# Kernel tuning notes

Hardware: AMD Instinct MI355X
Metric: run time of the kernel (lower is better)

## Reference

```python
import jax, jax.numpy as jnp
import numpy as np

# Fixed MANO structural constants (from MANO_RIGHT.pkl)
PARENTS = np.array([-1, 0, 1, 2, 0, 4, 5, 0, 7, 8, 0, 10, 11, 0, 13, 14])
FINGERTIP = np.array([745, 333, 444, 555, 672])
REMAP = np.array([0, 13, 14, 15, 16, 1, 2, 3, 17, 4, 5, 6, 18, 10, 11, 12, 19, 7, 8, 9, 20])
NV, NJ, NB, NP = 778, 16, 10, 135  # verts, joints, shape betas, pose-basis dim


def setup_inputs() -> dict:
    key = jax.random.key(0)
    ks = jax.random.split(key, 9)
    B = 8192
    beta = jax.random.normal(ks[0], (B, NB), jnp.float32)
    pose = jax.random.normal(ks[1], (B, NJ - 1, 3), jnp.float32) * 0.3
    rvec = jax.random.normal(ks[2], (B, 3), jnp.float32) * 0.3
    tvec = jax.random.normal(ks[3], (B, 3), jnp.float32)
    V = jax.random.normal(ks[4], (NV, 3), jnp.float32) * 0.1          # v_template
    S = jax.random.normal(ks[5], (NV, 3, NB), jnp.float32) * 0.01     # shapedirs
    P = jax.random.normal(ks[6], (NP, NV * 3), jnp.float32) * 0.01    # posedirs (reshaped, transposed)
    J_reg = jax.random.uniform(ks[7], (NJ, NV), jnp.float32)
    J_reg = J_reg / jnp.sum(J_reg, axis=-1, keepdims=True)
    W = jax.random.uniform(ks[8], (NV, NJ), jnp.float32)
    W = W / jnp.sum(W, axis=-1, keepdims=True)                        # skinning weights
    return {"beta": beta, "pose": pose, "rvec": rvec, "tvec": tvec,
            "V": V, "S": S, "P": P, "J_reg": J_reg, "W": W}


def _rodrigues(r):
    # r: [..., 3] axis-angle -> [..., 3, 3] rotation matrices
    sq = jnp.sum(r * r, axis=-1, keepdims=True)
    angle = jnp.sqrt(sq + 1e-8)
    axis = r / angle
    cos = jnp.cos(angle)[..., None]
    sin = jnp.sin(angle)[..., None]
    x, y, z = axis[..., 0], axis[..., 1], axis[..., 2]
    zeros = jnp.zeros_like(x)
    K = jnp.stack([zeros, -z, y, z, zeros, -x, -y, x, zeros], axis=-1)
    K = K.reshape(r.shape[:-1] + (3, 3))
    outer = axis[..., :, None] * axis[..., None, :]
    eye = jnp.eye(3, dtype=r.dtype)
    return cos * eye + (1.0 - cos) * outer + sin * K


def reference(beta, pose, rvec, tvec, V, S, P, J_reg, W):
    B = beta.shape[0]
    dtype = beta.dtype
    full_pose = jnp.concatenate([rvec[:, None, :], pose], axis=1)          # [B,16,3]
    # shape blendshapes
    v_shaped = V + jnp.einsum('bl,vkl->bvk', beta, S)                      # [B,778,3]
    Jrest = jnp.einsum('jv,bvk->bjk', J_reg, v_shaped)                     # [B,16,3]
    # pose blendshapes
    rot = _rodrigues(full_pose)                                            # [B,16,3,3]
    pose_feat = (rot[:, 1:] - jnp.eye(3, dtype=dtype)).reshape(B, NP)      # [B,135]
    v_posed = v_shaped + jnp.matmul(pose_feat, P).reshape(B, NV, 3)        # [B,778,3]
    # rigid transforms along the kinematic chain
    rel = Jrest.at[:, 1:].add(-Jrest[:, PARENTS[1:]])                      # parent-relative joint offsets
    T = jnp.zeros((B, NJ, 4, 4), dtype=dtype)
    T = T.at[..., :3, :3].set(rot).at[..., :3, 3].set(rel).at[..., 3, 3].set(1.0)
    chain = [T[:, 0]]
    for i in range(1, NJ):
        chain.append(jnp.matmul(chain[int(PARENTS[i])], T[:, i]))
    A = jnp.stack(chain, axis=1)                                           # [B,16,4,4] world transforms
    posed_joints = A[..., :3, 3]                                           # [B,16,3]
    # relative-to-rest transforms: A_rel = A - pad(A @ [Jrest;0])
    corr = jnp.einsum('bjmn,bjn->bjm', A[..., :3, :3], Jrest)
    A_rel = A.at[..., :3, 3].add(-corr)
    # linear blend skinning
    Tv = jnp.einsum('vj,bjmn->bvmn', W, A_rel)                             # [B,778,4,4]
    verts = jnp.einsum('bvmn,bvn->bvm', Tv[..., :3, :3], v_posed) + Tv[..., :3, 3]
    # 16 joints + 5 fingertips, remapped to 21 joints
    joints = jnp.concatenate([posed_joints, verts[:, FINGERTIP]], axis=1)[:, REMAP]
    verts = verts + tvec[:, None, :]
    joints = joints + tvec[:, None, :]
    return verts, joints
```

## Files before the change

kernel.cpp:

```cpp
#include <hip/hip_runtime.h>
#include <hip/hip_bf16.h>

typedef __attribute__((ext_vector_type(8))) short short8v;
typedef __attribute__((ext_vector_type(4))) float float4v;

#define BATCH 8192
#define NVERT 778
#define NJOINT 16
#define NPOSE 135
#define KEXT  160
#define NVT   52

#define WSB_JS    0u
#define WSB_PFX   4096u
#define WSB_A     (WSB_PFX  + 2621440u)
#define WSB_PTXF  (WSB_A    + 6291456u)
#define WSB_WF    (WSB_PTXF + 798720u)
#define WSB_ATF   (WSB_WF   + 53248u)

__global__ __launch_bounds__(256) void prep_kernel(
    const float* __restrict__ S, const float* __restrict__ V,
    const float* __restrict__ J_reg, const float* __restrict__ P,
    const float* __restrict__ W,
    float* __restrict__ wsJS, __hip_bfloat16* __restrict__ PtxF,
    __hip_bfloat16* __restrict__ WF)
{
    if (blockIdx.x < 132) {
        int o = blockIdx.x * 4 + (threadIdx.x >> 6);
        int lane = threadIdx.x & 63;
        float s = 0.f;
        if (o < 480) {
            int j = o / 30, k = (o / 10) % 3, l = o % 10;
            for (int v = lane; v < NVERT; v += 64)
                s += J_reg[j * NVERT + v] * S[v * 30 + k * 10 + l];
        } else if (o < 528) {
            int o2 = o - 480;
            int j = o2 / 3, k = o2 % 3;
            for (int v = lane; v < NVERT; v += 64)
                s += J_reg[j * NVERT + v] * V[v * 3 + k];
        }
#pragma unroll
        for (int m = 32; m >= 1; m >>= 1) s += __shfl_xor(s, m, 64);
        if (lane == 0 && o < 528) wsJS[o] = s;
        return;
    }

    int idx = (blockIdx.x - 132) * 256 + threadIdx.x;
    if (idx < NVT * 3 * 5 * 64) {
        int vt = idx / 960;
        int rem = idx % 960;
        int k = rem / 320;
        int rem2 = rem % 320;
        int kc = rem2 / 64;
        int lane = rem2 % 64;
        int v = vt * 16 + (lane & 15);
        int kbase = kc * 32 + (lane >> 4) * 8;
        short8v out;
#pragma unroll
        for (int jj = 0; jj < 8; ++jj) {
            int kk = kbase + jj;
            float val = 0.f;
            if (v < NVERT) {
                if (kk < NPOSE)            val = P[(size_t)kk * (NVERT * 3) + v * 3 + k];
                else if (kk < NPOSE + 10)  val = S[v * 30 + k * 10 + (kk - NPOSE)];
                else if (kk == NPOSE + 10) val = V[v * 3 + k];
            }
            __hip_bfloat16 h = __float2bfloat16(val);
            out[jj] = *reinterpret_cast<short*>(&h);
        }
        ((short8v*)PtxF)[idx] = out;
    } else if (idx < NVT * 3 * 5 * 64 + NVT * 64) {
        int t = idx - NVT * 3 * 5 * 64;
        int vt = t / 64, lane = t % 64;
        int v = vt * 16 + (lane & 15);
        int jbase = (lane >> 4) * 8;
        short8v out;
#pragma unroll
        for (int jj = 0; jj < 8; ++jj) {
            int j = jbase + jj;
            float val = (j < 16 && v < NVERT) ? W[v * 16 + j] : 0.f;
            __hip_bfloat16 h = __float2bfloat16(val);
            out[jj] = *reinterpret_cast<short*>(&h);
        }
        ((short8v*)WF)[t] = out;
    }
}

__device__ __forceinline__ void rodrigues(float x, float y, float z, float R[9])
{
    float sq = x * x + y * y + z * z;
    float angle = sqrtf(sq + 1e-8f);
    float inv = 1.0f / angle;
    float ax = x * inv, ay = y * inv, az = z * inv;
    float c = cosf(angle), s = sinf(angle);
    float ic = 1.0f - c;
    R[0] = c + ic * ax * ax;      R[1] = ic * ax * ay - s * az; R[2] = ic * ax * az + s * ay;
    R[3] = ic * ax * ay + s * az; R[4] = c + ic * ay * ay;      R[5] = ic * ay * az - s * ax;
    R[6] = ic * ax * az - s * ay; R[7] = ic * ay * az + s * ax; R[8] = c + ic * az * az;
}

__device__ __forceinline__ void writeATF(
    __hip_bfloat16* __restrict__ ATF, int b, int i,
    const float R[9], const float t[3], const float J[3])
{
    int bt = b >> 4;
    int lane32 = ((i >> 3) << 4) + (b & 15);
    size_t base = (((size_t)bt * 12) * 32 + lane32) * 8 + (i & 7);
    float vals[12];
#pragma unroll
    for (int m = 0; m < 3; ++m) {
        vals[m * 4 + 0] = R[m * 3 + 0];
        vals[m * 4 + 1] = R[m * 3 + 1];
        vals[m * 4 + 2] = R[m * 3 + 2];
        vals[m * 4 + 3] = t[m] - (R[m * 3 + 0] * J[0] + R[m * 3 + 1] * J[1] + R[m * 3 + 2] * J[2]);
    }
#pragma unroll
    for (int mn = 0; mn < 12; ++mn)
        ATF[base + (size_t)mn * 256] = __float2bfloat16(vals[mn]);
}

__global__ __launch_bounds__(256) void chain_kernel(
    const float* __restrict__ beta, const float* __restrict__ pose,
    const float* __restrict__ rvec, const float* __restrict__ tvec,
    const float* __restrict__ wsJS, __hip_bfloat16* __restrict__ pfx,
    __hip_bfloat16* __restrict__ ATF, float* __restrict__ out_joints)
{
    int t = blockIdx.x * 256 + threadIdx.x;
    int c = t >> 13;
    int b = t & (BATCH - 1);
    if (c >= 5) return;

    const int INVMAP[16] = {0, 5, 6, 7, 9, 10, 11, 17, 18, 19, 13, 14, 15, 1, 2, 3};

    float bt[10];
#pragma unroll
    for (int l = 0; l < 10; ++l) bt[l] = beta[b * 10 + l];

    float Jr0[3], Jrc[3][3];
#pragma unroll
    for (int k = 0; k < 3; ++k) {
        float s = wsJS[480 + k];
#pragma unroll
        for (int l = 0; l < 10; ++l) s += wsJS[k * 10 + l] * bt[l];
        Jr0[k] = s;
    }
#pragma unroll
    for (int sI = 0; sI < 3; ++sI) {
        int j = 3 * c + 1 + sI;
#pragma unroll
        for (int k = 0; k < 3; ++k) {
            float s = wsJS[480 + j * 3 + k];
#pragma unroll
            for (int l = 0; l < 10; ++l) s += wsJS[(j * 3 + k) * 10 + l] * bt[l];
            Jrc[sI][k] = s;
        }
    }

    float tv[3] = {tvec[b * 3 + 0], tvec[b * 3 + 1], tvec[b * 3 + 2]};

    float R0[9];
    rodrigues(rvec[b * 3 + 0], rvec[b * 3 + 1], rvec[b * 3 + 2], R0);
    float t0[3] = {Jr0[0], Jr0[1], Jr0[2]};

    __hip_bfloat16* pfb = pfx + (size_t)b * KEXT;
    float* jout = out_joints + (size_t)b * 63;

    if (c == 0) {
#pragma unroll
        for (int l = 0; l < 10; ++l) pfb[NPOSE + l] = __float2bfloat16(bt[l]);
        pfb[NPOSE + 10] = __float2bfloat16(1.0f);
#pragma unroll
        for (int l = NPOSE + 11; l < KEXT; ++l) pfb[l] = __float2bfloat16(0.0f);

#pragma unroll
        for (int k = 0; k < 3; ++k) jout[INVMAP[0] * 3 + k] = t0[k] + tv[k];
        writeATF(ATF, b, 0, R0, t0, Jr0);
    }

    float Rc[9], tc[3], prevJ[3];
#pragma unroll
    for (int q = 0; q < 9; ++q) Rc[q] = R0[q];
#pragma unroll
    for (int k = 0; k < 3; ++k) { tc[k] = t0[k]; prevJ[k] = Jr0[k]; }

#pragma unroll
    for (int s = 0; s < 3; ++s) {
        int i = 3 * c + 1 + s;
        float Ri[9];
        rodrigues(pose[b * 45 + (i - 1) * 3 + 0],
                  pose[b * 45 + (i - 1) * 3 + 1],
                  pose[b * 45 + (i - 1) * 3 + 2], Ri);
#pragma unroll
        for (int mn = 0; mn < 9; ++mn)
            pfb[(i - 1) * 9 + mn] =
                __float2bfloat16(Ri[mn] - ((mn == 0 || mn == 4 || mn == 8) ? 1.0f : 0.0f));

        float rel[3];
#pragma unroll
        for (int k = 0; k < 3; ++k) rel[k] = Jrc[s][k] - prevJ[k];

        float Rn[9], tn[3];
#pragma unroll
        for (int m = 0; m < 3; ++m) {
#pragma unroll
            for (int n = 0; n < 3; ++n)
                Rn[m * 3 + n] = Rc[m * 3 + 0] * Ri[0 + n] + Rc[m * 3 + 1] * Ri[3 + n] + Rc[m * 3 + 2] * Ri[6 + n];
            tn[m] = Rc[m * 3 + 0] * rel[0] + Rc[m * 3 + 1] * rel[1] + Rc[m * 3 + 2] * rel[2] + tc[m];
        }
#pragma unroll
        for (int q = 0; q < 9; ++q) Rc[q] = Rn[q];
#pragma unroll
        for (int k = 0; k < 3; ++k) { tc[k] = tn[k]; prevJ[k] = Jrc[s][k]; }

#pragma unroll
        for (int k = 0; k < 3; ++k) jout[INVMAP[i] * 3 + k] = tc[k] + tv[k];

        writeATF(ATF, b, i, Rc, tc, Jrc[s]);
    }
}

__device__ __forceinline__ void stage_tile(
    const __hip_bfloat16* __restrict__ PtxF,
    const __hip_bfloat16* __restrict__ WF,
    int vt, short* dst, int wave, int lane)
{
#pragma unroll
    for (int c = 0; c < 4; ++c) {
        int g = wave * 4 + c;
        const char* src = (g < 15)
            ? (const char*)PtxF + ((size_t)vt * 15 + g) * 1024
            : (const char*)WF + (size_t)vt * 1024;
        src += lane * 16;
        char* d = (char*)dst + g * 1024;
        __builtin_amdgcn_global_load_lds(
            (const __attribute__((address_space(1))) void*)src,
            (__attribute__((address_space(3))) void*)d,
            16, 0, 0);
    }
}

__global__ __launch_bounds__(256, 2) void verts_kernel(
    const __hip_bfloat16* __restrict__ pfx,
    const __hip_bfloat16* __restrict__ PtxF,
    const __hip_bfloat16* __restrict__ WF,
    const __hip_bfloat16* __restrict__ ATF,
    const float* __restrict__ tvec,
    float* __restrict__ out_verts, float* __restrict__ out_joints)
{
    __shared__ __align__(16) short Bs[2][16 * 64 * 8];

    int tid = threadIdx.x;
    int lane = tid & 63;
    int wave = tid >> 6;
    int l15 = lane & 15;
    int lg  = lane >> 4;

    int bt = blockIdx.x * 4 + wave;
    int b0 = bt * 16;
    int vg = blockIdx.y;

    int start = (vg == 0) ? 0 : 13 + (vg - 1) * 12;
    int count = (vg == 0) ? 13 : 12;

    short8v hA[5];
#pragma unroll
    for (int kc = 0; kc < 5; ++kc)
        hA[kc] = *(const short8v*)(pfx + (size_t)(b0 + l15) * KEXT + kc * 32 + lg * 8);

    short8v tA[12];
#pragma unroll
    for (int mn = 0; mn < 12; ++mn)
        tA[mn] = *(const short8v*)(ATF + (((size_t)bt * 12 + mn) * 32 + (lane & 31)) * 8);

    float tv[4][3];
#pragma unroll
    for (int r = 0; r < 4; ++r) {
        int b = b0 + lg * 4 + r;
#pragma unroll
        for (int m = 0; m < 3; ++m) tv[r][m] = tvec[b * 3 + m];
    }

    stage_tile(PtxF, WF, start, &Bs[0][0], wave, lane);
    asm volatile("s_waitcnt vmcnt(0)" ::: "memory");
    __builtin_amdgcn_s_barrier();
    __builtin_amdgcn_sched_barrier(0);

    for (int i = 0; i < count; ++i) {
        int vt = start + i;
        const short* cur = &Bs[i & 1][0];

        if (i + 1 < count)
            stage_tile(PtxF, WF, vt + 1, &Bs[(i + 1) & 1][0], wave, lane);
        __builtin_amdgcn_sched_barrier(0);

        short8v hB[15];
#pragma unroll
        for (int f = 0; f < 15; ++f)
            hB[f] = *(const short8v*)(cur + f * 512 + lane * 8);
        short8v wf = *(const short8v*)(cur + 15 * 512 + lane * 8);

        float4v hacc[3], Tacc[12];
#pragma unroll
        for (int k = 0; k < 3; ++k) hacc[k] = (float4v){0.f, 0.f, 0.f, 0.f};
#pragma unroll
        for (int mn = 0; mn < 12; ++mn) Tacc[mn] = (float4v){0.f, 0.f, 0.f, 0.f};

#pragma unroll
        for (int k = 0; k < 3; ++k)
#pragma unroll
            for (int kc = 0; kc < 5; ++kc)
                hacc[k] = __builtin_amdgcn_mfma_f32_16x16x32_bf16(
                    hA[kc], hB[k * 5 + kc], hacc[k], 0, 0, 0);

#pragma unroll
        for (int mn = 0; mn < 12; ++mn)
            Tacc[mn] = __builtin_amdgcn_mfma_f32_16x16x32_bf16(
                tA[mn], wf, Tacc[mn], 0, 0, 0);

        int v = vt * 16 + l15;
        int dest = (v == 745) ? 4 : (v == 333) ? 8 : (v == 444) ? 12 :
                   (v == 555) ? 16 : (v == 672) ? 20 : -1;

        if (v < NVERT) {
#pragma unroll
            for (int r = 0; r < 4; ++r) {
                float h0 = hacc[0][r], h1 = hacc[1][r], h2 = hacc[2][r];
                float e0 = Tacc[0][r] * h0 + Tacc[1][r] * h1 + Tacc[2][r]  * h2 + Tacc[3][r]  + tv[r][0];
                float e1 = Tacc[4][r] * h0 + Tacc[5][r] * h1 + Tacc[6][r]  * h2 + Tacc[7][r]  + tv[r][1];
                float e2 = Tacc[8][r] * h0 + Tacc[9][r] * h1 + Tacc[10][r] * h2 + Tacc[11][r] + tv[r][2];
                int b = b0 + lg * 4 + r;
                size_t idx = ((size_t)b * NVERT + v) * 3;
                out_verts[idx + 0] = e0;
                out_verts[idx + 1] = e1;
                out_verts[idx + 2] = e2;
                if (dest >= 0) {
                    size_t jidx = (size_t)b * 63 + dest * 3;
                    out_joints[jidx + 0] = e0;
                    out_joints[jidx + 1] = e1;
                    out_joints[jidx + 2] = e2;
                }
            }
        }

        if (i + 1 < count) {
            asm volatile("s_waitcnt vmcnt(4)" ::: "memory");
            __builtin_amdgcn_s_barrier();
            __builtin_amdgcn_sched_barrier(0);
        }
    }
}

extern "C" void kernel_launch(void* const* d_in, const int* in_sizes, int n_in,
                              void* d_out, int out_size, void* d_ws, size_t ws_size,
                              hipStream_t stream)
{
    const float* beta  = (const float*)d_in[0];
    const float* pose  = (const float*)d_in[1];
    const float* rvec  = (const float*)d_in[2];
    const float* tvec  = (const float*)d_in[3];
    const float* V     = (const float*)d_in[4];
    const float* S     = (const float*)d_in[5];
    const float* P     = (const float*)d_in[6];
    const float* J_reg = (const float*)d_in[7];
    const float* W     = (const float*)d_in[8];

    float* out    = (float*)d_out;
    float* verts  = out;
    float* joints = out + (size_t)BATCH * NVERT * 3;

    char* wsb = (char*)d_ws;
    float*          wsJS = (float*)(wsb + WSB_JS);
    __hip_bfloat16* pfx  = (__hip_bfloat16*)(wsb + WSB_PFX);
    __hip_bfloat16* PtxF = (__hip_bfloat16*)(wsb + WSB_PTXF);
    __hip_bfloat16* WFp  = (__hip_bfloat16*)(wsb + WSB_WF);
    __hip_bfloat16* ATF  = (__hip_bfloat16*)(wsb + WSB_ATF);

    hipLaunchKernelGGL(prep_kernel, dim3(340), dim3(256), 0, stream,
                       S, V, J_reg, P, W, wsJS, PtxF, WFp);
    hipLaunchKernelGGL(chain_kernel, dim3(160), dim3(256), 0, stream,
                       beta, pose, rvec, tvec, wsJS, pfx, ATF, joints);
    hipLaunchKernelGGL(verts_kernel, dim3(128, 4), dim3(256), 0, stream,
                       pfx, PtxF, WFp, ATF, tvec, verts, joints);
}
```

Before: 42.69 us.

## Rebalance kernel split, fold translation into transforms, double vertex-group grid

Moves the posedirs/weights packing out of the prep kernel and into the chain kernel launch, leaving a small standalone joint-regressor kernel, so that packing overlaps the chain computation. The per-batch translation is folded into the transform translation column, which removes the tvec loads and adds from the verts kernel. The verts kernel grid doubles to 8 vertex groups of about 6 tiles each, and launch bounds rise to 3 blocks per CU. The B-fragment loads are interleaved with the MFMAs to cut register pressure. Adding tvec before the bf16 conversion of the translation column may cost some precision.

```diff
diff --git a/kernel.cpp b/kernel.cpp
--- a/kernel.cpp
+++ b/kernel.cpp
@@ -18,72 +18,26 @@
 #define WSB_WF    (WSB_PTXF + 798720u)
 #define WSB_ATF   (WSB_WF   + 53248u)
 
-__global__ __launch_bounds__(256) void prep_kernel(
+__global__ __launch_bounds__(256) void js_kernel(
     const float* __restrict__ S, const float* __restrict__ V,
-    const float* __restrict__ J_reg, const float* __restrict__ P,
-    const float* __restrict__ W,
-    float* __restrict__ wsJS, __hip_bfloat16* __restrict__ PtxF,
-    __hip_bfloat16* __restrict__ WF)
-{
-    if (blockIdx.x < 132) {
-        int o = blockIdx.x * 4 + (threadIdx.x >> 6);
-        int lane = threadIdx.x & 63;
-        float s = 0.f;
-        if (o < 480) {
-            int j = o / 30, k = (o / 10) % 3, l = o % 10;
-            for (int v = lane; v < NVERT; v += 64)
-                s += J_reg[j * NVERT + v] * S[v * 30 + k * 10 + l];
-        } else if (o < 528) {
-            int o2 = o - 480;
-            int j = o2 / 3, k = o2 % 3;
-            for (int v = lane; v < NVERT; v += 64)
-                s += J_reg[j * NVERT + v] * V[v * 3 + k];
-        }
-#pragma unroll
-        for (int m = 32; m >= 1; m >>= 1) s += __shfl_xor(s, m, 64);
-        if (lane == 0 && o < 528) wsJS[o] = s;
-        return;
-    }
-
-    int idx = (blockIdx.x - 132) * 256 + threadIdx.x;
-    if (idx < NVT * 3 * 5 * 64) {
-        int vt = idx / 960;
-        int rem = idx % 960;
-        int k = rem / 320;
-        int rem2 = rem % 320;
-        int kc = rem2 / 64;
-        int lane = rem2 % 64;
-        int v = vt * 16 + (lane & 15);
-        int kbase = kc * 32 + (lane >> 4) * 8;
-        short8v out;
-#pragma unroll
-        for (int jj = 0; jj < 8; ++jj) {
-            int kk = kbase + jj;
-            float val = 0.f;
-            if (v < NVERT) {
-                if (kk < NPOSE)            val = P[(size_t)kk * (NVERT * 3) + v * 3 + k];
-                else if (kk < NPOSE + 10)  val = S[v * 30 + k * 10 + (kk - NPOSE)];
-                else if (kk == NPOSE + 10) val = V[v * 3 + k];
-            }
-            __hip_bfloat16 h = __float2bfloat16(val);
-            out[jj] = *reinterpret_cast<short*>(&h);
-        }
-        ((short8v*)PtxF)[idx] = out;
-    } else if (idx < NVT * 3 * 5 * 64 + NVT * 64) {
-        int t = idx - NVT * 3 * 5 * 64;
-        int vt = t / 64, lane = t % 64;
-        int v = vt * 16 + (lane & 15);
-        int jbase = (lane >> 4) * 8;
-        short8v out;
-#pragma unroll
-        for (int jj = 0; jj < 8; ++jj) {
-            int j = jbase + jj;
-            float val = (j < 16 && v < NVERT) ? W[v * 16 + j] : 0.f;
-            __hip_bfloat16 h = __float2bfloat16(val);
-            out[jj] = *reinterpret_cast<short*>(&h);
-        }
-        ((short8v*)WF)[t] = out;
-    }
+    const float* __restrict__ J_reg, float* __restrict__ wsJS)
+{
+    int o = blockIdx.x * 4 + (threadIdx.x >> 6);
+    int lane = threadIdx.x & 63;
+    float s = 0.f;
+    if (o < 480) {
+        int j = o / 30, k = (o / 10) % 3, l = o % 10;
+        for (int v = lane; v < NVERT; v += 64)
+            s += J_reg[j * NVERT + v] * S[v * 30 + k * 10 + l];
+    } else if (o < 528) {
+        int o2 = o - 480;
+        int j = o2 / 3, k = o2 % 3;
+        for (int v = lane; v < NVERT; v += 64)
+            s += J_reg[j * NVERT + v] * V[v * 3 + k];
+    }
+#pragma unroll
+    for (int m = 32; m >= 1; m >>= 1) s += __shfl_xor(s, m, 64);
+    if (lane == 0 && o < 528) wsJS[o] = s;
 }
 
 __device__ __forceinline__ void rodrigues(float x, float y, float z, float R[9])
@@ -101,7 +55,7 @@
 
 __device__ __forceinline__ void writeATF(
     __hip_bfloat16* __restrict__ ATF, int b, int i,
-    const float R[9], const float t[3], const float J[3])
+    const float R[9], const float t[3], const float J[3], const float tv[3])
 {
     int bt = b >> 4;
     int lane32 = ((i >> 3) << 4) + (b & 15);
@@ -112,20 +66,67 @@
         vals[m * 4 + 0] = R[m * 3 + 0];
         vals[m * 4 + 1] = R[m * 3 + 1];
         vals[m * 4 + 2] = R[m * 3 + 2];
-        vals[m * 4 + 3] = t[m] - (R[m * 3 + 0] * J[0] + R[m * 3 + 1] * J[1] + R[m * 3 + 2] * J[2]);
+        vals[m * 4 + 3] = t[m] + tv[m] - (R[m * 3 + 0] * J[0] + R[m * 3 + 1] * J[1] + R[m * 3 + 2] * J[2]);
     }
 #pragma unroll
     for (int mn = 0; mn < 12; ++mn)
         ATF[base + (size_t)mn * 256] = __float2bfloat16(vals[mn]);
 }
 
-__global__ __launch_bounds__(256) void chain_kernel(
+__global__ __launch_bounds__(256) void buildchain_kernel(
+    const float* __restrict__ S, const float* __restrict__ V,
+    const float* __restrict__ P, const float* __restrict__ W,
     const float* __restrict__ beta, const float* __restrict__ pose,
     const float* __restrict__ rvec, const float* __restrict__ tvec,
-    const float* __restrict__ wsJS, __hip_bfloat16* __restrict__ pfx,
-    __hip_bfloat16* __restrict__ ATF, float* __restrict__ out_joints)
-{
-    int t = blockIdx.x * 256 + threadIdx.x;
+    const float* __restrict__ wsJS,
+    __hip_bfloat16* __restrict__ PtxF, __hip_bfloat16* __restrict__ WF,
+    __hip_bfloat16* __restrict__ pfx, __hip_bfloat16* __restrict__ ATF,
+    float* __restrict__ out_joints)
+{
+    if (blockIdx.x < 208) {
+        int idx = blockIdx.x * 256 + threadIdx.x;
+        if (idx < NVT * 3 * 5 * 64) {
+            int vt = idx / 960;
+            int rem = idx % 960;
+            int k = rem / 320;
+            int rem2 = rem % 320;
+            int kc = rem2 / 64;
+            int lane = rem2 % 64;
+            int v = vt * 16 + (lane & 15);
+            int kbase = kc * 32 + (lane >> 4) * 8;
+            short8v out;
+#pragma unroll
+            for (int jj = 0; jj < 8; ++jj) {
+                int kk = kbase + jj;
+                float val = 0.f;
+                if (v < NVERT) {
+                    if (kk < NPOSE)            val = P[(size_t)kk * (NVERT * 3) + v * 3 + k];
+                    else if (kk < NPOSE + 10)  val = S[v * 30 + k * 10 + (kk - NPOSE)];
+                    else if (kk == NPOSE + 10) val = V[v * 3 + k];
+                }
+                __hip_bfloat16 h = __float2bfloat16(val);
+                out[jj] = *reinterpret_cast<short*>(&h);
+            }
+            ((short8v*)PtxF)[idx] = out;
+        } else if (idx < NVT * 3 * 5 * 64 + NVT * 64) {
+            int t = idx - NVT * 3 * 5 * 64;
+            int vt = t / 64, lane = t % 64;
+            int v = vt * 16 + (lane & 15);
+            int jbase = (lane >> 4) * 8;
+            short8v out;
+#pragma unroll
+            for (int jj = 0; jj < 8; ++jj) {
+                int j = jbase + jj;
+                float val = (j < 16 && v < NVERT) ? W[v * 16 + j] : 0.f;
+                __hip_bfloat16 h = __float2bfloat16(val);
+                out[jj] = *reinterpret_cast<short*>(&h);
+            }
+            ((short8v*)WF)[t] = out;
+        }
+        return;
+    }
+
+    int t = (blockIdx.x - 208) * 256 + threadIdx.x;
     int c = t >> 13;
     int b = t & (BATCH - 1);
     if (c >= 5) return;
@@ -174,7 +175,7 @@
 
 #pragma unroll
         for (int k = 0; k < 3; ++k) jout[INVMAP[0] * 3 + k] = t0[k] + tv[k];
-        writeATF(ATF, b, 0, R0, t0, Jr0);
+        writeATF(ATF, b, 0, R0, t0, Jr0, tv);
     }
 
     float Rc[9], tc[3], prevJ[3];
@@ -215,7 +216,7 @@
 #pragma unroll
         for (int k = 0; k < 3; ++k) jout[INVMAP[i] * 3 + k] = tc[k] + tv[k];
 
-        writeATF(ATF, b, i, Rc, tc, Jrc[s]);
+        writeATF(ATF, b, i, Rc, tc, Jrc[s], tv);
     }
 }
 
@@ -239,12 +240,11 @@
     }
 }
 
-__global__ __launch_bounds__(256, 2) void verts_kernel(
+__global__ __launch_bounds__(256, 3) void verts_kernel(
     const __hip_bfloat16* __restrict__ pfx,
     const __hip_bfloat16* __restrict__ PtxF,
     const __hip_bfloat16* __restrict__ WF,
     const __hip_bfloat16* __restrict__ ATF,
-    const float* __restrict__ tvec,
     float* __restrict__ out_verts, float* __restrict__ out_joints)
 {
     __shared__ __align__(16) short Bs[2][16 * 64 * 8];
@@ -259,8 +259,8 @@
     int b0 = bt * 16;
     int vg = blockIdx.y;
 
-    int start = (vg == 0) ? 0 : 13 + (vg - 1) * 12;
-    int count = (vg == 0) ? 13 : 12;
+    int start = (vg == 0) ? 0 : 7 + (vg - 1) * 6;
+    int count = (vg == 0) ? 7 : 6;
 
     short8v hA[5];
 #pragma unroll
@@ -271,14 +271,6 @@
 #pragma unroll
     for (int mn = 0; mn < 12; ++mn)
         tA[mn] = *(const short8v*)(ATF + (((size_t)bt * 12 + mn) * 32 + (lane & 31)) * 8);
-
-    float tv[4][3];
-#pragma unroll
-    for (int r = 0; r < 4; ++r) {
-        int b = b0 + lg * 4 + r;
-#pragma unroll
-        for (int m = 0; m < 3; ++m) tv[r][m] = tvec[b * 3 + m];
-    }
 
     stage_tile(PtxF, WF, start, &Bs[0][0], wave, lane);
     asm volatile("s_waitcnt vmcnt(0)" ::: "memory");
@@ -293,25 +285,19 @@
             stage_tile(PtxF, WF, vt + 1, &Bs[(i + 1) & 1][0], wave, lane);
         __builtin_amdgcn_sched_barrier(0);
 
-        short8v hB[15];
-#pragma unroll
-        for (int f = 0; f < 15; ++f)
-            hB[f] = *(const short8v*)(cur + f * 512 + lane * 8);
+        float4v hacc[3], Tacc[12];
+#pragma unroll
+        for (int k = 0; k < 3; ++k) hacc[k] = (float4v){0.f, 0.f, 0.f, 0.f};
+#pragma unroll
+        for (int mn = 0; mn < 12; ++mn) Tacc[mn] = (float4v){0.f, 0.f, 0.f, 0.f};
+
+#pragma unroll
+        for (int f = 0; f < 15; ++f) {
+            short8v hB = *(const short8v*)(cur + f * 512 + lane * 8);
+            hacc[f / 5] = __builtin_amdgcn_mfma_f32_16x16x32_bf16(
+                hA[f % 5], hB, hacc[f / 5], 0, 0, 0);
+        }
         short8v wf = *(const short8v*)(cur + 15 * 512 + lane * 8);
-
-        float4v hacc[3], Tacc[12];
-#pragma unroll
-        for (int k = 0; k < 3; ++k) hacc[k] = (float4v){0.f, 0.f, 0.f, 0.f};
-#pragma unroll
-        for (int mn = 0; mn < 12; ++mn) Tacc[mn] = (float4v){0.f, 0.f, 0.f, 0.f};
-
-#pragma unroll
-        for (int k = 0; k < 3; ++k)
-#pragma unroll
-            for (int kc = 0; kc < 5; ++kc)
-                hacc[k] = __builtin_amdgcn_mfma_f32_16x16x32_bf16(
-                    hA[kc], hB[k * 5 + kc], hacc[k], 0, 0, 0);
-
 #pragma unroll
         for (int mn = 0; mn < 12; ++mn)
             Tacc[mn] = __builtin_amdgcn_mfma_f32_16x16x32_bf16(
@@ -325,9 +311,9 @@
 #pragma unroll
             for (int r = 0; r < 4; ++r) {
                 float h0 = hacc[0][r], h1 = hacc[1][r], h2 = hacc[2][r];
-                float e0 = Tacc[0][r] * h0 + Tacc[1][r] * h1 + Tacc[2][r]  * h2 + Tacc[3][r]  + tv[r][0];
-                float e1 = Tacc[4][r] * h0 + Tacc[5][r] * h1 + Tacc[6][r]  * h2 + Tacc[7][r]  + tv[r][1];
-                float e2 = Tacc[8][r] * h0 + Tacc[9][r] * h1 + Tacc[10][r] * h2 + Tacc[11][r] + tv[r][2];
+                float e0 = Tacc[0][r] * h0 + Tacc[1][r] * h1 + Tacc[2][r]  * h2 + Tacc[3][r];
+                float e1 = Tacc[4][r] * h0 + Tacc[5][r] * h1 + Tacc[6][r]  * h2 + Tacc[7][r];
+                float e2 = Tacc[8][r] * h0 + Tacc[9][r] * h1 + Tacc[10][r] * h2 + Tacc[11][r];
                 int b = b0 + lg * 4 + r;
                 size_t idx = ((size_t)b * NVERT + v) * 3;
                 out_verts[idx + 0] = e0;
@@ -375,10 +361,11 @@
     __hip_bfloat16* WFp  = (__hip_bfloat16*)(wsb + WSB_WF);
     __hip_bfloat16* ATF  = (__hip_bfloat16*)(wsb + WSB_ATF);
 
-    hipLaunchKernelGGL(prep_kernel, dim3(340), dim3(256), 0, stream,
-                       S, V, J_reg, P, W, wsJS, PtxF, WFp);
-    hipLaunchKernelGGL(chain_kernel, dim3(160), dim3(256), 0, stream,
-                       beta, pose, rvec, tvec, wsJS, pfx, ATF, joints);
-    hipLaunchKernelGGL(verts_kernel, dim3(128, 4), dim3(256), 0, stream,
-                       pfx, PtxF, WFp, ATF, tvec, verts, joints);
-}
+    hipLaunchKernelGGL(js_kernel, dim3(132), dim3(256), 0, stream,
+                       S, V, J_reg, wsJS);
+    hipLaunchKernelGGL(buildchain_kernel, dim3(368), dim3(256), 0, stream,
+                       S, V, P, W, beta, pose, rvec, tvec, wsJS,
+                       PtxF, WFp, pfx, ATF, joints);
+    hipLaunchKernelGGL(verts_kernel, dim3(128, 8), dim3(256), 0, stream,
+                       pfx, PtxF, WFp, ATF, verts, joints);
+}
```

Result: slower. 48.74 us (+14.2%).
